# Optimization experiments

Hardware: AMD Instinct MI355X
Metric: run time of the kernel (lower is better)

The kernel has to match this reference:

```python
import jax, jax.numpy as jnp
import numpy as np

P = 16          # patch_size
C = 3           # in_chans
D = 768         # embed_dim
V = 10240       # position_embedding_size
B, H, W = 16, 512, 512
N = (H // P) * (W // P)  # 1024 patches per image


def setup_inputs() -> dict:
    key = jax.random.key(0)
    k1, k2, k3, k4, k5 = jax.random.split(key, 5)
    pixel_values = jax.random.uniform(k1, (B, C, H, W), dtype=jnp.float32)
    position_ids = jax.random.randint(k2, (B, N, 2), 0, 32)  # (x, y) patch coords < pW/pH
    padding_positions = jax.random.randint(k3, (B, N), 0, 2).astype(jnp.bool_)
    w_proj = jax.random.normal(k4, (D, C * P * P), dtype=jnp.float32) * 0.02  # Linear weight (out, in)
    pos_table = jax.random.normal(k5, (2, V, D), dtype=jnp.float32) * 0.02
    return {
        "pixel_values": pixel_values,
        "w_proj": w_proj,
        "pos_table": pos_table,
        "position_ids": position_ids,
        "padding_positions": padding_positions,
    }


def reference(pixel_values, w_proj, pos_table, position_ids, padding_positions):
    b, c, h, w = pixel_values.shape
    ph, pw = h // P, w // P
    # Extract patches in Gemma4 C-P-P flatten order: (B, N, C*P*P)
    x = pixel_values.reshape(b, c, ph, P, pw, P)
    x = jnp.transpose(x, (0, 2, 4, 1, 3, 5)).reshape(b, ph * pw, c * P * P)
    patches = 2.0 * (x - 0.5)
    hidden = jnp.einsum('bnf,df->bnd', patches, w_proj)
    # Position embeddings: one_hot(ids) @ table summed over the 2 axes
    # == direct gather-add: table[0][x_id] + table[1][y_id]
    ids = jnp.clip(position_ids, 0)
    pos = pos_table[0][ids[..., 0]] + pos_table[1][ids[..., 1]]  # (B, N, D)
    pos = jnp.where(padding_positions[..., None], 0.0, pos)
    return hidden + pos
```

## Files before the change

### kernel.cpp

```cpp
#include <hip/hip_runtime.h>
#include <stdint.h>


typedef __attribute__((ext_vector_type(8))) short bfrag_t;
typedef __attribute__((ext_vector_type(16))) float f16acc;
typedef __attribute__((ext_vector_type(8))) unsigned short u16x8;
typedef __attribute__((ext_vector_type(4))) unsigned short u16x4;

#define V_POS 10240
#define RSA 776

__device__ __forceinline__ unsigned short f2bf(float f) {
    unsigned int u = __float_as_uint(f);
    u += 0x7fffu + ((u >> 16) & 1u);
    return (unsigned short)(u >> 16);
}

__global__ __launch_bounds__(256) void bpack_kernel(
    const float* __restrict__ wp, unsigned short* __restrict__ Bp)
{
    int u     = blockIdx.x * 256 + threadIdx.x;
    int chunk = u >> 6;
    int lane  = u & 63;
    int n32   = chunk / 48;
    int k16   = chunk - n32 * 48;
    int n     = (n32 << 5) + (lane & 31);
    int k     = (k16 << 4) + ((lane >> 5) << 3);
    const float* s = wp + (size_t)n * 768 + k;
    float4 v0 = *(const float4*)s;
    float4 v1 = *(const float4*)(s + 4);
    u16x8 o;
    o[0] = f2bf(v0.x); o[1] = f2bf(v0.y); o[2] = f2bf(v0.z); o[3] = f2bf(v0.w);
    o[4] = f2bf(v1.x); o[5] = f2bf(v1.y); o[6] = f2bf(v1.z); o[7] = f2bf(v1.w);
    *(u16x8*)(Bp + (size_t)chunk * 512 + (lane << 3)) = o;
}

__global__ __launch_bounds__(512, 4) void fused_kernel(
    const float* __restrict__ px, const unsigned short* __restrict__ Bp,
    const int* __restrict__ pos_ids, const unsigned int* __restrict__ pad_in,
    const float* __restrict__ pos_table, float* __restrict__ out)
{
    __shared__ unsigned short As[32 * RSA];

    const int tid  = threadIdx.x;
    const int wave = tid >> 6;
    const int lane = tid & 63;
    const int bid  = blockIdx.x;
    const int m0   = bid << 5;
    const int img  = bid >> 5;
    const int prow = bid & 31;

    const float* base = px + ((size_t)img * 3 * 512 + (size_t)prow * 16) * 512;
#pragma unroll 6
    for (int it = 0; it < 12; ++it) {
        int idx = it * 512 + tid;
        int c   = idx >> 11;
        int rem = idx & 2047;
        int hl  = rem >> 7;
        int w4  = rem & 127;
        float4 v = *(const float4*)(base + (size_t)c * 262144 + hl * 512 + (w4 << 2));
        int r = w4 >> 2;
        int k = (c << 8) + (hl << 4) + ((w4 & 3) << 2);
        u16x4 o;
        o[0] = f2bf(2.f * v.x - 1.f);
        o[1] = f2bf(2.f * v.y - 1.f);
        o[2] = f2bf(2.f * v.z - 1.f);
        o[3] = f2bf(2.f * v.w - 1.f);
        *(u16x4*)&As[r * RSA + k] = o;
    }
    __syncthreads();

    const bool u8mode = __any(pad_in[lane] > 1u);

    const unsigned short* afrag = As + (size_t)(lane & 31) * RSA + ((lane >> 5) << 3);
    const unsigned short* bbase = Bp + (size_t)(wave * 3) * 48 * 512 + (lane << 3);

    f16acc acc[3] = {};

    bfrag_t aC, bC0, bC1, bC2;
    bfrag_t aN, bN0, bN1, bN2;

#define LDA(k, r0) { r0 = *(const bfrag_t*)(afrag + ((k) << 4)); }
#define LDB(k, r0, r1, r2) { const unsigned short* bk_ = bbase + (size_t)(k) * 512; \
        r0 = *(const bfrag_t*)(bk_);                                          \
        r1 = *(const bfrag_t*)(bk_ + 48 * 512);                               \
        r2 = *(const bfrag_t*)(bk_ + 96 * 512); }
#define MFMA3(a0, b0, b1, b2)                                                 \
        acc[0] = __builtin_amdgcn_mfma_f32_32x32x16_bf16(a0, b0, acc[0], 0, 0, 0); \
        acc[1] = __builtin_amdgcn_mfma_f32_32x32x16_bf16(a0, b1, acc[1], 0, 0, 0); \
        acc[2] = __builtin_amdgcn_mfma_f32_32x32x16_bf16(a0, b2, acc[2], 0, 0, 0);

    LDA(0, aC); LDB(0, bC0, bC1, bC2);
    LDA(1, aN); LDB(1, bN0, bN1, bN2);

    for (int k16 = 0; k16 < 48; k16 += 2) {
        MFMA3(aC, bC0, bC1, bC2);
        if (k16 + 2 < 48) { LDA(k16 + 2, aC); LDB(k16 + 2, bC0, bC1, bC2); }
        MFMA3(aN, bN0, bN1, bN2);
        if (k16 + 3 < 48) { LDA(k16 + 3, aN); LDB(k16 + 3, bN0, bN1, bN2); }
    }
#undef LDA
#undef LDB
#undef MFMA3

    const unsigned char* pad8 = (const unsigned char*)pad_in;
    const int cl  = lane & 31;
    const int h4  = (lane >> 5) << 2;
#pragma unroll 4
    for (int r = 0; r < 16; ++r) {
        int row = (r & 3) + ((r >> 2) << 3) + h4;
        int gm  = m0 + row;
        int xid = pos_ids[2 * gm];
        int yid = pos_ids[2 * gm + 1];
        xid = xid < 0 ? 0 : xid;
        yid = yid < 0 ? 0 : yid;
        bool p = u8mode ? (pad8[gm] != 0) : (pad_in[gm] != 0u);
        const float* t0 = pos_table + (size_t)xid * 768;
        const float* t1 = pos_table + (size_t)(V_POS + yid) * 768;
        float* orow = out + (size_t)gm * 768;
#pragma unroll
        for (int nt = 0; nt < 3; ++nt) {
            int col = wave * 96 + (nt << 5) + cl;
            float pos = p ? 0.f : (t0[col] + t1[col]);
            orow[col] = acc[nt][r] + pos;
        }
    }
}

extern "C" void kernel_launch(void* const* d_in, const int* in_sizes, int n_in,
                              void* d_out, int out_size, void* d_ws, size_t ws_size,
                              hipStream_t stream) {
    const float*        px  = (const float*)d_in[0];
    const float*        wp  = (const float*)d_in[1];
    const float*        pt  = (const float*)d_in[2];
    const int*          pid = (const int*)d_in[3];
    const unsigned int* pad = (const unsigned int*)d_in[4];

    unsigned short* Bp = (unsigned short*)d_ws;

    bpack_kernel<<<288, 256, 0, stream>>>(wp, Bp);
    fused_kernel<<<512, 512, 0, stream>>>(px, Bp, pid, pad, pt, (float*)d_out);
}
```

Measured before the change: 174.1 us.

## Load A fragments directly from global pixels, drop LDS staging

Removes the shared-memory staging of the patch tile and its barrier. Each wave now loads its A fragments straight from global pixel memory, converting to bf16 in registers inside the software-pipelined MFMA loop. It also adds nontemporal loads for B and nontemporal stores for the output, and fully unrolls the epilogue. In exchange, every one of the 8 waves re-reads the same pixel data from global/L2 memory instead of sharing it once through LDS, and the conversion work is repeated per wave.

```diff
diff --git a/kernel.cpp b/kernel.cpp
--- a/kernel.cpp
+++ b/kernel.cpp
@@ -1,14 +1,13 @@
 #include <hip/hip_runtime.h>
+#include <hip/hip_bf16.h>
 #include <stdint.h>
 
 
 typedef __attribute__((ext_vector_type(8))) short bfrag_t;
 typedef __attribute__((ext_vector_type(16))) float f16acc;
 typedef __attribute__((ext_vector_type(8))) unsigned short u16x8;
-typedef __attribute__((ext_vector_type(4))) unsigned short u16x4;
 
 #define V_POS 10240
-#define RSA 776
 
 __device__ __forceinline__ unsigned short f2bf(float f) {
     unsigned int u = __float_as_uint(f);
@@ -40,8 +39,6 @@
     const int* __restrict__ pos_ids, const unsigned int* __restrict__ pad_in,
     const float* __restrict__ pos_table, float* __restrict__ out)
 {
-    __shared__ unsigned short As[32 * RSA];
-
     const int tid  = threadIdx.x;
     const int wave = tid >> 6;
     const int lane = tid & 63;
@@ -50,63 +47,59 @@
     const int img  = bid >> 5;
     const int prow = bid & 31;
 
-    const float* base = px + ((size_t)img * 3 * 512 + (size_t)prow * 16) * 512;
-#pragma unroll 6
-    for (int it = 0; it < 12; ++it) {
-        int idx = it * 512 + tid;
-        int c   = idx >> 11;
-        int rem = idx & 2047;
-        int hl  = rem >> 7;
-        int w4  = rem & 127;
-        float4 v = *(const float4*)(base + (size_t)c * 262144 + hl * 512 + (w4 << 2));
-        int r = w4 >> 2;
-        int k = (c << 8) + (hl << 4) + ((w4 & 3) << 2);
-        u16x4 o;
-        o[0] = f2bf(2.f * v.x - 1.f);
-        o[1] = f2bf(2.f * v.y - 1.f);
-        o[2] = f2bf(2.f * v.z - 1.f);
-        o[3] = f2bf(2.f * v.w - 1.f);
-        *(u16x4*)&As[r * RSA + k] = o;
-    }
-    __syncthreads();
+    const int col8 = ((lane & 31) << 4) + ((lane >> 5) << 3);
+    const float* pxb = px + (size_t)img * 786432 + (size_t)(prow * 16) * 512 + col8;
+    const unsigned short* bbase = Bp + (size_t)(wave * 3) * 48 * 512 + (lane << 3);
 
     const bool u8mode = __any(pad_in[lane] > 1u);
 
-    const unsigned short* afrag = As + (size_t)(lane & 31) * RSA + ((lane >> 5) << 3);
-    const unsigned short* bbase = Bp + (size_t)(wave * 3) * 48 * 512 + (lane << 3);
-
     f16acc acc[3] = {};
 
-    bfrag_t aC, bC0, bC1, bC2;
-    bfrag_t aN, bN0, bN1, bN2;
+    float4  aCr0, aCr1, aNr0, aNr1;
+    bfrag_t bC0, bC1, bC2, bN0, bN1, bN2;
 
-#define LDA(k, r0) { r0 = *(const bfrag_t*)(afrag + ((k) << 4)); }
-#define LDB(k, r0, r1, r2) { const unsigned short* bk_ = bbase + (size_t)(k) * 512; \
-        r0 = *(const bfrag_t*)(bk_);                                          \
-        r1 = *(const bfrag_t*)(bk_ + 48 * 512);                               \
-        r2 = *(const bfrag_t*)(bk_ + 96 * 512); }
+#define LOADA(k, r0, r1) { \
+        const float* a_ = pxb + ((k) >> 4) * 262144 + ((k) & 15) * 512; \
+        r0 = *(const float4*)a_; r1 = *(const float4*)(a_ + 4); }
+#define LOADB(k, r0, r1, r2) { \
+        const unsigned short* bk_ = bbase + (size_t)(k) * 512; \
+        r0 = __builtin_nontemporal_load((const bfrag_t*)bk_); \
+        r1 = __builtin_nontemporal_load((const bfrag_t*)(bk_ + 48 * 512)); \
+        r2 = __builtin_nontemporal_load((const bfrag_t*)(bk_ + 96 * 512)); }
+#define CVT(r0, r1, dst) { \
+        union { bfrag_t v; __hip_bfloat162 h[4]; } u_; \
+        u_.h[0] = __float22bfloat162_rn(make_float2(fmaf(2.f, r0.x, -1.f), fmaf(2.f, r0.y, -1.f))); \
+        u_.h[1] = __float22bfloat162_rn(make_float2(fmaf(2.f, r0.z, -1.f), fmaf(2.f, r0.w, -1.f))); \
+        u_.h[2] = __float22bfloat162_rn(make_float2(fmaf(2.f, r1.x, -1.f), fmaf(2.f, r1.y, -1.f))); \
+        u_.h[3] = __float22bfloat162_rn(make_float2(fmaf(2.f, r1.z, -1.f), fmaf(2.f, r1.w, -1.f))); \
+        dst = u_.v; }
 #define MFMA3(a0, b0, b1, b2)                                                 \
         acc[0] = __builtin_amdgcn_mfma_f32_32x32x16_bf16(a0, b0, acc[0], 0, 0, 0); \
         acc[1] = __builtin_amdgcn_mfma_f32_32x32x16_bf16(a0, b1, acc[1], 0, 0, 0); \
         acc[2] = __builtin_amdgcn_mfma_f32_32x32x16_bf16(a0, b2, acc[2], 0, 0, 0);
 
-    LDA(0, aC); LDB(0, bC0, bC1, bC2);
-    LDA(1, aN); LDB(1, bN0, bN1, bN2);
+    LOADA(0, aCr0, aCr1); LOADB(0, bC0, bC1, bC2);
+    LOADA(1, aNr0, aNr1); LOADB(1, bN0, bN1, bN2);
 
-    for (int k16 = 0; k16 < 48; k16 += 2) {
+    for (int k16 = 0; k16 < 46; k16 += 2) {
+        bfrag_t aC; CVT(aCr0, aCr1, aC);
         MFMA3(aC, bC0, bC1, bC2);
-        if (k16 + 2 < 48) { LDA(k16 + 2, aC); LDB(k16 + 2, bC0, bC1, bC2); }
+        LOADA(k16 + 2, aCr0, aCr1); LOADB(k16 + 2, bC0, bC1, bC2);
+        bfrag_t aN; CVT(aNr0, aNr1, aN);
         MFMA3(aN, bN0, bN1, bN2);
-        if (k16 + 3 < 48) { LDA(k16 + 3, aN); LDB(k16 + 3, bN0, bN1, bN2); }
+        if (k16 + 3 < 48) { LOADA(k16 + 3, aNr0, aNr1); LOADB(k16 + 3, bN0, bN1, bN2); }
     }
-#undef LDA
-#undef LDB
+    { bfrag_t aC; CVT(aCr0, aCr1, aC); MFMA3(aC, bC0, bC1, bC2); }
+    { bfrag_t aN; CVT(aNr0, aNr1, aN); MFMA3(aN, bN0, bN1, bN2); }
+#undef LOADA
+#undef LOADB
+#undef CVT
 #undef MFMA3
 
     const unsigned char* pad8 = (const unsigned char*)pad_in;
     const int cl  = lane & 31;
     const int h4  = (lane >> 5) << 2;
-#pragma unroll 4
+#pragma unroll
     for (int r = 0; r < 16; ++r) {
         int row = (r & 3) + ((r >> 2) << 3) + h4;
         int gm  = m0 + row;
@@ -122,7 +115,7 @@
         for (int nt = 0; nt < 3; ++nt) {
             int col = wave * 96 + (nt << 5) + cl;
             float pos = p ? 0.f : (t0[col] + t1[col]);
-            orow[col] = acc[nt][r] + pos;
+            __builtin_nontemporal_store(acc[nt][r] + pos, &orow[col]);
         }
     }
 }
```

New measurement: 538.8 us. 209% more time.
